# Performance work log

Hardware: AMD Instinct MI355X
Metric: run time of the kernel (lower is better)

## Reference

```python
import jax, jax.numpy as jnp
import numpy as np

N, E, FIN, H, G, L = 100000, 300000, 128, 256, 4000, 5
BN_EPS = 1e-5

def setup_inputs() -> dict:
    key = jax.random.key(0)
    ks = jax.random.split(key, 24)
    s = 0.05
    inp = {
        "x": jax.random.normal(ks[0], (N, FIN), dtype=jnp.float32),
        "edge_index": jax.random.randint(ks[1], (2, E), 0, N, dtype=jnp.int64),
        "batch": jnp.sort(jax.random.randint(ks[2], (N,), 0, G, dtype=jnp.int64)),
        # input projection
        "in_W": jax.random.normal(ks[3], (FIN, H), dtype=jnp.float32) * s,
        "in_b": jnp.zeros((H,), dtype=jnp.float32),
        # stacked per-layer GIN MLP params (Linear-BN-ReLU-Linear-BN-ReLU)
        "conv_W1": jax.random.normal(ks[4], (L, H, H), dtype=jnp.float32) * s,
        "conv_b1": jnp.zeros((L, H), dtype=jnp.float32),
        "conv_g1": jnp.ones((L, H), dtype=jnp.float32),
        "conv_be1": jnp.zeros((L, H), dtype=jnp.float32),
        "conv_W2": jax.random.normal(ks[5], (L, H, H), dtype=jnp.float32) * s,
        "conv_b2": jnp.zeros((L, H), dtype=jnp.float32),
        "conv_g2": jnp.ones((L, H), dtype=jnp.float32),
        "conv_be2": jnp.zeros((L, H), dtype=jnp.float32),
        "eps": jnp.zeros((L,), dtype=jnp.float32),
        # head MLP
        "head_W1": jax.random.normal(ks[6], (H, H // 2), dtype=jnp.float32) * s,
        "head_b1": jnp.zeros((H // 2,), dtype=jnp.float32),
        "head_W2": jax.random.normal(ks[7], (H // 2, 1), dtype=jnp.float32) * s,
        "head_b2": jnp.zeros((1,), dtype=jnp.float32),
    }
    return inp

def _bn(h, g, b):
    # BatchNorm1d over node dim (training-mode batch stats)
    m = jnp.mean(h, axis=0)
    v = jnp.var(h, axis=0)
    return g * (h - m) * jax.lax.rsqrt(v + BN_EPS) + b

def reference(x, edge_index, batch, in_W, in_b, conv_W1, conv_b1, conv_g1,
              conv_be1, conv_W2, conv_b2, conv_g2, conv_be2, eps,
              head_W1, head_b1, head_W2, head_b2):
    src, dst = edge_index[0], edge_index[1]
    h = jax.nn.relu(x @ in_W + in_b)  # [N,H]
    for l in range(L):
        agg = jax.ops.segment_sum(h[src], dst, num_segments=N)  # scatter-add
        z = (1.0 + eps[l]) * h + agg
        z = jax.nn.relu(_bn(z @ conv_W1[l] + conv_b1[l], conv_g1[l], conv_be1[l]))
        h = jax.nn.relu(_bn(z @ conv_W2[l] + conv_b2[l], conv_g2[l], conv_be2[l]))
        # dropout is identity in eval/reference
    # global mean pool by graph id
    sums = jax.ops.segment_sum(h, batch, num_segments=G)  # [G,H]
    cnt = jax.ops.segment_sum(jnp.ones((N,), h.dtype), batch, num_segments=G)
    pooled = sums / jnp.maximum(cnt, 1.0)[:, None]
    hid = jax.nn.relu(pooled @ head_W1 + head_b1)
    return hid @ head_W2 + head_b2  # [G,1]
```

## Files before the change

kernel.cpp:

```cpp
#include <hip/hip_runtime.h>
#include <hip/hip_bf16.h>
#include <stdint.h>
#include <stddef.h>

#define NN 100000
#define NE 300000
#define FINDIM 128
#define HD 256
#define NG 4000
#define NLAYER 5
#define MPAD 100096
#define NT (MPAD/32)
#define MG 384

typedef __attribute__((ext_vector_type(8))) short bf8;
typedef __attribute__((ext_vector_type(4))) float f4;

#define FENCE() __asm__ volatile("" ::: "memory")
#define WAITVM0() __asm__ volatile("s_waitcnt vmcnt(0)" ::: "memory")
#define WAITVM4() __asm__ volatile("s_waitcnt vmcnt(4)" ::: "memory")
#define WAITVM6() __asm__ volatile("s_waitcnt vmcnt(6)" ::: "memory")
#define WAITLGKM() __asm__ volatile("s_waitcnt lgkmcnt(0)" ::: "memory")
#define BARRIER() do { FENCE(); __builtin_amdgcn_s_barrier(); FENCE(); } while(0)

__device__ __forceinline__ unsigned short f2bf(float f){
  union { float f; unsigned u; } uf; uf.f = f;
  unsigned r = uf.u + 0x7fffu + ((uf.u >> 16) & 1u);
  return (unsigned short)(r >> 16);
}
__device__ __forceinline__ float bf2f(unsigned short h){
  union { unsigned u; float f; } uf; uf.u = ((unsigned)h) << 16; return uf.f;
}

__device__ __forceinline__ void gload16(const void* g, void* l){
  __builtin_amdgcn_global_load_lds((const __attribute__((address_space(1))) void*)g,
                                   (__attribute__((address_space(3))) void*)l, 16, 0, 0);
}

__global__ void k_zero(int* __restrict__ p, int n){
  int i = blockIdx.x*256 + threadIdx.x;
  if(i < n) p[i] = 0;
}

__global__ void k_count(const int* __restrict__ ei, int* __restrict__ counts){
  int e = blockIdx.x*256 + threadIdx.x;
  if(e < NE) atomicAdd(&counts[ei[NE + e]], 1);
}

__global__ void k_scan_partial(const int* __restrict__ counts, int* __restrict__ partials){
  __shared__ int sw[4];
  int b = blockIdx.x, t = threadIdx.x;
  int base = b*1024 + t*4;
  int s = 0;
  #pragma unroll
  for(int j=0;j<4;j++){ int i = base+j; if(i < NN) s += counts[i]; }
  #pragma unroll
  for(int d=1; d<64; d<<=1) s += __shfl_xor(s, d, 64);
  if((t & 63) == 0) sw[t>>6] = s;
  __syncthreads();
  if(t == 0) partials[b] = sw[0]+sw[1]+sw[2]+sw[3];
}

__global__ void k_scan_tot(int* __restrict__ partials, int* __restrict__ offsets, int nb){
  __shared__ int sm[128];
  int t = threadIdx.x;
  int v = (t < nb) ? partials[t] : 0;
  sm[t] = v; __syncthreads();
  for(int d=1; d<128; d<<=1){
    int x = 0;
    if(t >= d) x = sm[t-d];
    __syncthreads();
    sm[t] += x;
    __syncthreads();
  }
  if(t < nb) partials[t] = sm[t] - v;
  if(t == 127) offsets[NN] = sm[127];
}

__global__ void k_scan_final(const int* __restrict__ counts, const int* __restrict__ partials,
                             int* __restrict__ offsets, int* __restrict__ cursor){
  __shared__ int wsum[4];
  int b = blockIdx.x, t = threadIdx.x;
  int base = b*1024 + t*4;
  int c[4]; int ts = 0;
  #pragma unroll
  for(int j=0;j<4;j++){ int i = base+j; c[j] = (i < NN) ? counts[i] : 0; ts += c[j]; }
  int lane = t & 63;
  int inc = ts;
  #pragma unroll
  for(int d=1; d<64; d<<=1){ int x = __shfl_up(inc, d, 64); if(lane >= d) inc += x; }
  if(lane == 63) wsum[t>>6] = inc;
  __syncthreads();
  int woff = 0;
  for(int w2=0; w2<(t>>6); w2++) woff += wsum[w2];
  int excl = partials[b] + woff + inc - ts;
  #pragma unroll
  for(int j=0;j<4;j++){
    int i = base+j;
    if(i < NN){ offsets[i] = excl; cursor[i] = excl; excl += c[j]; }
  }
}

__global__ void k_fill(const int* __restrict__ ei, int* __restrict__ cursor, int* __restrict__ eidx){
  int e = blockIdx.x*256 + threadIdx.x;
  if(e < NE){
    int d = ei[NE + e];
    int pos = atomicAdd(&cursor[d], 1);
    eidx[pos] = ei[e];
  }
}

__global__ void k_wt(const float* __restrict__ src, unsigned short* __restrict__ dst, int K, int Ncols){
  int l = blockIdx.y;
  size_t base = (size_t)l * K * Ncols;
  int i = blockIdx.x*256 + threadIdx.x;
  if(i < K*Ncols){
    int k = i / Ncols, n = i % Ncols;
    dst[base + (size_t)n*K + k] = f2bf(src[base + i]);
  }
}

template<int TRANS, bool RELUOUT, bool STATS>
__global__ __launch_bounds__(256, 3) void k_gemmb(
    const unsigned short* __restrict__ A, const unsigned short* __restrict__ Bt,
    const float* __restrict__ bias, const float* __restrict__ preS,
    const float* __restrict__ preT, unsigned short* __restrict__ C,
    float* __restrict__ stats)
{
  __shared__ __align__(16) unsigned short As[2][8192];
  __shared__ __align__(16) unsigned short Cs[4][1152];
  __shared__ __align__(16) float SP[512];
  const int t = threadIdx.x;
  const int lane = t & 63, w = t >> 6;
  const int q = lane >> 4, ln = lane & 15;
  const int nh = blockIdx.x & 1;
  const int mg = blockIdx.x >> 1;
  const int nbase = nh*128 + w*32;

  if(TRANS){ SP[t] = preS[t]; SP[256 + t] = preT[t]; WAITLGKM(); }

  bf8 bb[2][8];
  #pragma unroll
  for(int nf=0; nf<2; nf++)
    #pragma unroll
    for(int s=0; s<8; s++)
      bb[nf][s] = *(const bf8*)(Bt + (size_t)(nbase + nf*16 + ln)*HD + s*32 + q*8);

  float bv[2];
  #pragma unroll
  for(int nf=0; nf<2; nf++) bv[nf] = bias[nbase + nf*16 + ln];

  auto issueA = [&](int mt, int b){
    const int m0 = mt*32;
    #pragma unroll
    for(int j=0; j<4; j++){
      int slot = j*256 + t;
      int row = slot >> 5, p = slot & 31;
      int c = p ^ (row & 7);
      gload16(A + (size_t)(m0 + row)*HD + c*8, &As[b][(j*256 + w*64)*8]);
    }
  };

  float sacc[2] = {0.f, 0.f}, ssacc[2] = {0.f, 0.f};

  issueA(mg, 0);
  issueA(mg + MG, 1);

  int tc = 0;
  for(int mt = mg; mt < NT; mt += MG, tc++){
    const bool last = (mt + MG >= NT);
    if(last)           WAITVM0();
    else if(tc == 0)   WAITVM4();
    else               WAITVM6();
    BARRIER();

    unsigned short* Ab = &As[tc&1][0];
    const int m0 = mt*32;
    const bool padt = (m0 >= NN);

    if(TRANS){
      #pragma unroll
      for(int j=0; j<4; j++){
        int slot = j*256 + t;
        if(padt){
          *(uint4*)&Ab[slot*8] = (uint4){0u,0u,0u,0u};
        } else {
          int row = slot >> 5, p = slot & 31;
          int c = p ^ (row & 7);
          uint4 u = *(const uint4*)&Ab[slot*8];
          f4 s0 = *(const f4*)&SP[c*8];
          f4 s1 = *(const f4*)&SP[c*8 + 4];
          f4 t0 = *(const f4*)&SP[256 + c*8];
          f4 t1 = *(const f4*)&SP[256 + c*8 + 4];
          float scv[8] = {s0.x,s0.y,s0.z,s0.w,s1.x,s1.y,s1.z,s1.w};
          float shv[8] = {t0.x,t0.y,t0.z,t0.w,t1.x,t1.y,t1.z,t1.w};
          unsigned short* us = (unsigned short*)&u;
          #pragma unroll
          for(int e=0; e<8; e++){
            float v = bf2f(us[e]);
            v = fmaxf(fmaf(scv[e], v, shv[e]), 0.f);
            us[e] = f2bf(v);
          }
          *(uint4*)&Ab[slot*8] = u;
        }
      }
      WAITLGKM();
      BARRIER();
    }

    f4 acc[2][2];
    #pragma unroll
    for(int i=0;i<2;i++)
      #pragma unroll
      for(int j=0;j<2;j++) acc[i][j] = (f4){0.f,0.f,0.f,0.f};

    #pragma unroll
    for(int s=0; s<8; s++){
      bf8 af[2];
      #pragma unroll
      for(int mi=0; mi<2; mi++){
        int row = mi*16 + ln;
        int p = (s*4 + q) ^ (row & 7);
        af[mi] = *(const bf8*)&Ab[row*256 + p*8];
      }
      #pragma unroll
      for(int mi=0; mi<2; mi++)
        #pragma unroll
        for(int nf=0; nf<2; nf++)
          acc[mi][nf] = __builtin_amdgcn_mfma_f32_16x16x32_bf16(af[mi], bb[nf][s], acc[mi][nf], 0, 0, 0);
    }

    if(STATS){
      #pragma unroll
      for(int nf=0; nf<2; nf++)
        #pragma unroll
        for(int mi=0; mi<2; mi++)
          #pragma unroll
          for(int r=0; r<4; r++){
            float v = acc[mi][nf][r];
            sacc[nf] += v; ssacc[nf] = fmaf(v, v, ssacc[nf]);
          }
    }

    unsigned short* wsc = &Cs[w][0];
    #pragma unroll
    for(int mi=0; mi<2; mi++)
      #pragma unroll
      for(int nf=0; nf<2; nf++)
        #pragma unroll
        for(int r=0; r<4; r++){
          float v = acc[mi][nf][r] + bv[nf];
          if(RELUOUT) v = fmaxf(v, 0.f);
          if(padt) v = 0.f;
          wsc[(mi*16 + q*4 + r)*36 + nf*16 + ln] = f2bf(v);
        }
    {
      int r2 = lane >> 1, ch = lane & 1;
      size_t cb = (size_t)(m0 + r2)*HD + nh*128 + w*32;
      uint4 u0 = *(const uint4*)&wsc[r2*36 + ch*8];
      uint4 u1 = *(const uint4*)&wsc[r2*36 + (ch+2)*8];
      *(uint4*)&C[cb + ch*8]     = u0;
      *(uint4*)&C[cb + (ch+2)*8] = u1;
    }

    WAITLGKM();
    BARRIER();
    if(mt + 2*MG < NT) issueA(mt + 2*MG, tc&1);
  }

  if(STATS){
    #pragma unroll
    for(int nf=0; nf<2; nf++){
      float s = sacc[nf], ss = ssacc[nf];
      s  += __shfl_xor(s, 16, 64);  s  += __shfl_xor(s, 32, 64);
      ss += __shfl_xor(ss, 16, 64); ss += __shfl_xor(ss, 32, 64);
      if(q == 0){
        int gn = nbase + nf*16 + ln;
        atomicAdd(&stats[gn], s);
        atomicAdd(&stats[HD + gn], ss);
      }
    }
  }
}

__global__ __launch_bounds__(256, 3) void k_gemmb_in(
    const float* __restrict__ A, const unsigned short* __restrict__ Bt,
    const float* __restrict__ bias, unsigned short* __restrict__ C)
{
  __shared__ __align__(16) unsigned short As[4096];
  __shared__ __align__(16) unsigned short Cs[4][1152];
  const int t = threadIdx.x;
  const int lane = t & 63, w = t >> 6;
  const int q = lane >> 4, ln = lane & 15;
  const int nh = blockIdx.x & 1;
  const int mg = blockIdx.x >> 1;
  const int nbase = nh*128 + w*32;

  bf8 bb[2][4];
  #pragma unroll
  for(int nf=0; nf<2; nf++)
    #pragma unroll
    for(int s=0; s<4; s++)
      bb[nf][s] = *(const bf8*)(Bt + (size_t)(nbase + nf*16 + ln)*FINDIM + s*32 + q*8);

  float bv[2];
  #pragma unroll
  for(int nf=0; nf<2; nf++) bv[nf] = bias[nbase + nf*16 + ln];

  for(int mt = mg; mt < NT; mt += MG){
    const int m0 = mt*32;
    const bool padt = (m0 >= NN);
    __syncthreads();
    #pragma unroll
    for(int j=0; j<2; j++){
      int slot = j*256 + t;
      int row = slot >> 4, p = slot & 15;
      int c = p ^ (row & 7);
      int gm = m0 + row;
      f4 v0 = (f4){0.f,0.f,0.f,0.f}, v1 = (f4){0.f,0.f,0.f,0.f};
      if(gm < NN){
        v0 = *(const f4*)&A[(size_t)gm*FINDIM + c*8];
        v1 = *(const f4*)&A[(size_t)gm*FINDIM + c*8 + 4];
      }
      ushort4 a0, a1;
      a0.x = f2bf(v0.x); a0.y = f2bf(v0.y); a0.z = f2bf(v0.z); a0.w = f2bf(v0.w);
      a1.x = f2bf(v1.x); a1.y = f2bf(v1.y); a1.z = f2bf(v1.z); a1.w = f2bf(v1.w);
      *(ushort4*)&As[row*128 + p*8]     = a0;
      *(ushort4*)&As[row*128 + p*8 + 4] = a1;
    }
    __syncthreads();

    f4 acc[2][2];
    #pragma unroll
    for(int i=0;i<2;i++)
      #pragma unroll
      for(int j=0;j<2;j++) acc[i][j] = (f4){0.f,0.f,0.f,0.f};

    #pragma unroll
    for(int s=0; s<4; s++){
      bf8 af[2];
      #pragma unroll
      for(int mi=0; mi<2; mi++){
        int row = mi*16 + ln;
        int p = (s*4 + q) ^ (row & 7);
        af[mi] = *(const bf8*)&As[row*128 + p*8];
      }
      #pragma unroll
      for(int mi=0; mi<2; mi++)
        #pragma unroll
        for(int nf=0; nf<2; nf++)
          acc[mi][nf] = __builtin_amdgcn_mfma_f32_16x16x32_bf16(af[mi], bb[nf][s], acc[mi][nf], 0, 0, 0);
    }

    unsigned short* wsc = &Cs[w][0];
    #pragma unroll
    for(int mi=0; mi<2; mi++)
      #pragma unroll
      for(int nf=0; nf<2; nf++)
        #pragma unroll
        for(int r=0; r<4; r++){
          float v = fmaxf(acc[mi][nf][r] + bv[nf], 0.f);
          if(padt) v = 0.f;
          wsc[(mi*16 + q*4 + r)*36 + nf*16 + ln] = f2bf(v);
        }
    int r2 = lane >> 1, ch = lane & 1;
    size_t cb = (size_t)(m0 + r2)*HD + nh*128 + w*32;
    uint4 u0 = *(const uint4*)&wsc[r2*36 + ch*8];
    uint4 u1 = *(const uint4*)&wsc[r2*36 + (ch+2)*8];
    *(uint4*)&C[cb + ch*8]     = u0;
    *(uint4*)&C[cb + (ch+2)*8] = u1;
  }
}

__global__ void k_bnfin(const float* __restrict__ cs, const float* __restrict__ bias,
                        const float* __restrict__ g, const float* __restrict__ be,
                        float* __restrict__ sc, float* __restrict__ sh){
  int c = threadIdx.x;
  float m0 = cs[c] * (1.0f/NN);
  float mean = m0 + bias[c];
  float var  = cs[HD + c] * (1.0f/NN) - m0*m0;
  float s = g[c] * rsqrtf(var + 1e-5f);
  sc[c] = s;
  sh[c] = be[c] - mean*s;
}

__device__ __forceinline__ f4 act4(ushort4 uv, f4 s4, f4 t4, int ident){
  f4 u;
  u.x = bf2f(uv.x); u.y = bf2f(uv.y); u.z = bf2f(uv.z); u.w = bf2f(uv.w);
  if(!ident){
    u.x = fmaxf(fmaf(s4.x, u.x, t4.x), 0.f);
    u.y = fmaxf(fmaf(s4.y, u.y, t4.y), 0.f);
    u.z = fmaxf(fmaf(s4.z, u.z, t4.z), 0.f);
    u.w = fmaxf(fmaf(s4.w, u.w, t4.w), 0.f);
  }
  return u;
}

__global__ __launch_bounds__(256) void k_agg(const unsigned short* __restrict__ src,
    unsigned short* __restrict__ dst,
    const int* __restrict__ offs, const int* __restrict__ eidx,
    const float* __restrict__ eps, int l,
    const float* __restrict__ sc, const float* __restrict__ sh, int ident)
{
  int wv = threadIdx.x >> 6;
  int n = blockIdx.x*4 + wv;
  if(n >= NN) return;
  int lane = threadIdx.x & 63;
  int c = lane << 2;
  f4 s4 = (f4){0.f,0.f,0.f,0.f}, t4 = (f4){0.f,0.f,0.f,0.f};
  if(!ident){ s4 = *(const f4*)(sc + c); t4 = *(const f4*)(sh + c); }
  float ep = 1.f + eps[l];
  f4 a = act4(*(const ushort4*)(src + (size_t)n*HD + c), s4, t4, ident);
  f4 acc;
  acc.x = ep*a.x; acc.y = ep*a.y; acc.z = ep*a.z; acc.w = ep*a.w;
  int lo = offs[n], hi = offs[n+1];
  for(int base = lo; base < hi; base += 64){
    int rem = hi - base; if(rem > 64) rem = 64;
    int idx = 0;
    if(base + lane < hi) idx = eidx[base + lane];
    int j = 0;
    for(; j + 4 <= rem; j += 4){
      int s0 = __shfl(idx, j, 64),   s1 = __shfl(idx, j+1, 64);
      int s2 = __shfl(idx, j+2, 64), s3 = __shfl(idx, j+3, 64);
      ushort4 u0 = *(const ushort4*)(src + (size_t)s0*HD + c);
      ushort4 u1 = *(const ushort4*)(src + (size_t)s1*HD + c);
      ushort4 u2 = *(const ushort4*)(src + (size_t)s2*HD + c);
      ushort4 u3 = *(const ushort4*)(src + (size_t)s3*HD + c);
      f4 a0 = act4(u0, s4, t4, ident), a1 = act4(u1, s4, t4, ident);
      f4 a2 = act4(u2, s4, t4, ident), a3 = act4(u3, s4, t4, ident);
      acc.x += (a0.x + a1.x) + (a2.x + a3.x);
      acc.y += (a0.y + a1.y) + (a2.y + a3.y);
      acc.z += (a0.z + a1.z) + (a2.z + a3.z);
      acc.w += (a0.w + a1.w) + (a2.w + a3.w);
    }
    for(; j < rem; j++){
      int s0 = __shfl(idx, j, 64);
      f4 a0 = act4(*(const ushort4*)(src + (size_t)s0*HD + c), s4, t4, ident);
      acc.x += a0.x; acc.y += a0.y; acc.z += a0.z; acc.w += a0.w;
    }
  }
  ushort4 o;
  o.x = f2bf(acc.x); o.y = f2bf(acc.y); o.z = f2bf(acc.z); o.w = f2bf(acc.w);
  *(ushort4*)(dst + (size_t)n*HD + c) = o;
}

__device__ __forceinline__ int lowb(const int* __restrict__ arr, int n, int key){
  int lo = 0, hi = n;
  while(lo < hi){ int mid = (lo + hi) >> 1; if(arr[mid] < key) lo = mid + 1; else hi = mid; }
  return lo;
}

__global__ __launch_bounds__(256) void k_pool(const unsigned short* __restrict__ src,
    const int* __restrict__ batch,
    const float* __restrict__ sc, const float* __restrict__ sh, float* __restrict__ pooled)
{
  int wv = threadIdx.x >> 6;
  int g = blockIdx.x*4 + wv;
  if(g >= NG) return;
  int lane = threadIdx.x & 63;
  int c = lane << 2;
  int lo = lowb(batch, NN, g);
  int hi = lowb(batch, NN, g+1);
  f4 s4 = *(const f4*)(sc + c);
  f4 t4 = *(const f4*)(sh + c);
  f4 acc = (f4){0.f,0.f,0.f,0.f};
  for(int n=lo; n<hi; n++){
    ushort4 uv = *(const ushort4*)(src + (size_t)n*HD + c);
    acc.x += fmaxf(fmaf(s4.x, bf2f(uv.x), t4.x), 0.f);
    acc.y += fmaxf(fmaf(s4.y, bf2f(uv.y), t4.y), 0.f);
    acc.z += fmaxf(fmaf(s4.z, bf2f(uv.z), t4.z), 0.f);
    acc.w += fmaxf(fmaf(s4.w, bf2f(uv.w), t4.w), 0.f);
  }
  float inv = 1.0f / fmaxf((float)(hi - lo), 1.0f);
  acc.x *= inv; acc.y *= inv; acc.z *= inv; acc.w *= inv;
  *(f4*)(pooled + (size_t)g*HD + c) = acc;
}

__global__ __launch_bounds__(128) void k_head(const float* __restrict__ pooled,
    const float* __restrict__ W1, const float* __restrict__ b1,
    const float* __restrict__ W2, const float* __restrict__ b2, float* __restrict__ out)
{
  __shared__ float p[HD];
  __shared__ float red[2];
  int g = blockIdx.x, t = threadIdx.x;
  if(t < 64) *(f4*)&p[t*4] = *(const f4*)(pooled + (size_t)g*HD + t*4);
  __syncthreads();
  float s = b1[t];
  for(int k=0;k<HD;k++) s = fmaf(p[k], W1[k*128 + t], s);
  float o = fmaxf(s, 0.f) * W2[t];
  #pragma unroll
  for(int d=1; d<64; d<<=1) o += __shfl_xor(o, d, 64);
  if((t & 63) == 0) red[t>>6] = o;
  __syncthreads();
  if(t == 0) out[g] = red[0] + red[1] + b2[0];
}

extern "C" void kernel_launch(void* const* d_in, const int* in_sizes, int n_in,
                              void* d_out, int out_size, void* d_ws, size_t ws_size,
                              hipStream_t stream) {
  const float* x    = (const float*)d_in[0];
  const int*   ei   = (const int*)  d_in[1];
  const int*   bat  = (const int*)  d_in[2];
  const float* inW  = (const float*)d_in[3];
  const float* inb  = (const float*)d_in[4];
  const float* W1   = (const float*)d_in[5];
  const float* b1   = (const float*)d_in[6];
  const float* g1   = (const float*)d_in[7];
  const float* be1  = (const float*)d_in[8];
  const float* W2   = (const float*)d_in[9];
  const float* b2   = (const float*)d_in[10];
  const float* g2   = (const float*)d_in[11];
  const float* be2  = (const float*)d_in[12];
  const float* eps  = (const float*)d_in[13];
  const float* hW1  = (const float*)d_in[14];
  const float* hb1  = (const float*)d_in[15];
  const float* hW2  = (const float*)d_in[16];
  const float* hb2  = (const float*)d_in[17];
  float* out = (float*)d_out;

  char* p = (char*)d_ws;
  auto alloc = [&](size_t bytes)->char*{
    char* r = p; p += (bytes + 255) & ~(size_t)255; return r;
  };
  unsigned short* B0 = (unsigned short*)alloc((size_t)MPAD*HD*2);
  unsigned short* B1 = (unsigned short*)alloc((size_t)MPAD*HD*2);
  unsigned short* Wtin = (unsigned short*)alloc((size_t)FINDIM*HD*2);
  unsigned short* Wt1  = (unsigned short*)alloc((size_t)NLAYER*HD*HD*2);
  unsigned short* Wt2  = (unsigned short*)alloc((size_t)NLAYER*HD*HD*2);
  int* counts  = (int*)alloc((size_t)NN*4);
  int* offsets = (int*)alloc((size_t)(NN+1)*4);
  int* cursor  = (int*)alloc((size_t)NN*4);
  int* eidx    = (int*)alloc((size_t)NE*4);
  int* partials= (int*)alloc(128*4);
  float* cs    = (float*)alloc(4*HD*4);
  float* bnp   = (float*)alloc(4*HD*4);
  float* pooled= (float*)alloc((size_t)NG*HD*4);

  k_zero<<<(NN+255)/256, 256, 0, stream>>>(counts, NN);
  k_count<<<(NE+255)/256, 256, 0, stream>>>(ei, counts);
  int nb = (NN + 1023)/1024;
  k_scan_partial<<<nb, 256, 0, stream>>>(counts, partials);
  k_scan_tot<<<1, 128, 0, stream>>>(partials, offsets, nb);
  k_scan_final<<<nb, 256, 0, stream>>>(counts, partials, offsets, cursor);
  k_fill<<<(NE+255)/256, 256, 0, stream>>>(ei, cursor, eidx);

  k_wt<<<dim3((FINDIM*HD+255)/256, 1), 256, 0, stream>>>(inW, Wtin, FINDIM, HD);
  k_wt<<<dim3((HD*HD+255)/256, NLAYER), 256, 0, stream>>>(W1, Wt1, HD, HD);
  k_wt<<<dim3((HD*HD+255)/256, NLAYER), 256, 0, stream>>>(W2, Wt2, HD, HD);

  {
    int padInts = (MPAD - NN) * HD / 2;
    k_zero<<<(padInts+255)/256, 256, 0, stream>>>((int*)(B1 + (size_t)NN*HD), padInts);
  }

  k_gemmb_in<<<2*MG, 256, 0, stream>>>(x, Wtin, inb, B0);

  float* sc1 = bnp, *sh1 = bnp + HD, *sc2 = bnp + 2*HD, *sh2 = bnp + 3*HD;
  unsigned short* hbuf = B0;
  unsigned short* tbuf = B1;
  for(int l=0; l<NLAYER; l++){
    k_zero<<<4, 256, 0, stream>>>((int*)cs, 4*HD);
    k_agg<<<(NN+3)/4, 256, 0, stream>>>(hbuf, tbuf, offsets, eidx, eps, l, sc2, sh2, l==0 ? 1 : 0);
    k_gemmb<0, false, true><<<2*MG, 256, 0, stream>>>(tbuf, Wt1 + (size_t)l*HD*HD, b1 + l*HD,
                                                      nullptr, nullptr, hbuf, cs);
    k_bnfin<<<1, HD, 0, stream>>>(cs, b1 + l*HD, g1 + l*HD, be1 + l*HD, sc1, sh1);
    k_gemmb<1, false, true><<<2*MG, 256, 0, stream>>>(hbuf, Wt2 + (size_t)l*HD*HD, b2 + l*HD,
                                                      sc1, sh1, tbuf, cs + 2*HD);
    k_bnfin<<<1, HD, 0, stream>>>(cs + 2*HD, b2 + l*HD, g2 + l*HD, be2 + l*HD, sc2, sh2);
    unsigned short* tmp = hbuf; hbuf = tbuf; tbuf = tmp;
  }

  k_pool<<<(NG+3)/4, 256, 0, stream>>>(hbuf, bat, sc2, sh2, pooled);
  k_head<<<NG, 128, 0, stream>>>(pooled, hW1, hb1, hW2, hb2, out);
}
```

Baseline: 840.5 us.

## Fuse neighbor aggregation into first GIN GEMM with gathered LDS tiles

Replaces the separate aggregation kernel and first per-layer GEMM with one kernel that gathers neighbor rows, applies the pending BN+ReLU, sums with (1+eps)·self, and writes the bf16 tile straight into shared memory. An MFMA GEMM over the full 256 output columns then runs on that tile, with 512-thread blocks and the whole weight slice held in registers. This removes the write and reread of the aggregated activation buffer in every layer. The cost is that the irregular gather latency now sits inside the GEMM loop, overlapped only by double buffering, and the larger register footprint may lower occupancy. The buffer ping-pong is replaced by fixed B0/B1 roles.

```diff
diff --git a/kernel.cpp b/kernel.cpp
--- a/kernel.cpp
+++ b/kernel.cpp
@@ -11,7 +11,8 @@
 #define NLAYER 5
 #define MPAD 100096
 #define NT (MPAD/32)
-#define MG 384
+#define MGB 384
+#define MGF 512
 
 typedef __attribute__((ext_vector_type(8))) short bf8;
 typedef __attribute__((ext_vector_type(4))) float f4;
@@ -117,6 +118,178 @@
   if(i < K*Ncols){
     int k = i / Ncols, n = i % Ncols;
     dst[base + (size_t)n*K + k] = f2bf(src[base + i]);
+  }
+}
+
+__device__ __forceinline__ f4 act4(ushort4 uv, f4 s4, f4 t4, int ident){
+  f4 u;
+  u.x = bf2f(uv.x); u.y = bf2f(uv.y); u.z = bf2f(uv.z); u.w = bf2f(uv.w);
+  if(!ident){
+    u.x = fmaxf(fmaf(s4.x, u.x, t4.x), 0.f);
+    u.y = fmaxf(fmaf(s4.y, u.y, t4.y), 0.f);
+    u.z = fmaxf(fmaf(s4.z, u.z, t4.z), 0.f);
+    u.w = fmaxf(fmaf(s4.w, u.w, t4.w), 0.f);
+  }
+  return u;
+}
+
+template<int IDENT>
+__global__ __launch_bounds__(512) void k_gfuse(
+    const unsigned short* __restrict__ h, const unsigned short* __restrict__ Bt,
+    const float* __restrict__ bias, const float* __restrict__ sc,
+    const float* __restrict__ sh, const float* __restrict__ eps, int l,
+    const int* __restrict__ offs, const int* __restrict__ eidx,
+    unsigned short* __restrict__ C, float* __restrict__ stats)
+{
+  __shared__ __align__(16) unsigned short As[2][8192];
+  __shared__ __align__(16) unsigned short Cs[8][1152];
+  const int t = threadIdx.x;
+  const int lane = t & 63, w = t >> 6;
+  const int q = lane >> 4, ln = lane & 15;
+  const int mg = blockIdx.x;
+  const int nbase = w*32;
+  const int gc = lane*4;
+
+  f4 s4 = (f4){0.f,0.f,0.f,0.f}, t4 = (f4){0.f,0.f,0.f,0.f};
+  if(!IDENT){ s4 = *(const f4*)(sc + gc); t4 = *(const f4*)(sh + gc); }
+  const float ep = 1.f + eps[l];
+
+  bf8 bb[2][8];
+  #pragma unroll
+  for(int nf=0; nf<2; nf++)
+    #pragma unroll
+    for(int s=0; s<8; s++)
+      bb[nf][s] = *(const bf8*)(Bt + (size_t)(nbase + nf*16 + ln)*HD + s*32 + q*8);
+
+  float bv[2];
+  #pragma unroll
+  for(int nf=0; nf<2; nf++) bv[nf] = bias[nbase + nf*16 + ln];
+
+  auto gather = [&](int mt, int b){
+    unsigned short* Ab = &As[b][0];
+    const int m0 = mt*32;
+    if(m0 >= NN){
+      *(uint4*)&Ab[t*16]     = (uint4){0u,0u,0u,0u};
+      *(uint4*)&Ab[t*16 + 8] = (uint4){0u,0u,0u,0u};
+      return;
+    }
+    #pragma unroll
+    for(int rr=0; rr<4; rr++){
+      const int r = w*4 + rr;
+      const int n = m0 + r;
+      f4 a = act4(*(const ushort4*)(h + (size_t)n*HD + gc), s4, t4, IDENT);
+      f4 acc;
+      acc.x = ep*a.x; acc.y = ep*a.y; acc.z = ep*a.z; acc.w = ep*a.w;
+      int lo = offs[n], hi = offs[n+1];
+      for(int base = lo; base < hi; base += 64){
+        int rem = hi - base; if(rem > 64) rem = 64;
+        int idxv = 0;
+        if(base + lane < hi) idxv = eidx[base + lane];
+        int j = 0;
+        for(; j + 4 <= rem; j += 4){
+          int s0 = __shfl(idxv, j, 64),   s1 = __shfl(idxv, j+1, 64);
+          int s2 = __shfl(idxv, j+2, 64), s3 = __shfl(idxv, j+3, 64);
+          ushort4 u0 = *(const ushort4*)(h + (size_t)s0*HD + gc);
+          ushort4 u1 = *(const ushort4*)(h + (size_t)s1*HD + gc);
+          ushort4 u2 = *(const ushort4*)(h + (size_t)s2*HD + gc);
+          ushort4 u3 = *(const ushort4*)(h + (size_t)s3*HD + gc);
+          f4 a0 = act4(u0, s4, t4, IDENT), a1 = act4(u1, s4, t4, IDENT);
+          f4 a2 = act4(u2, s4, t4, IDENT), a3 = act4(u3, s4, t4, IDENT);
+          acc.x += (a0.x + a1.x) + (a2.x + a3.x);
+          acc.y += (a0.y + a1.y) + (a2.y + a3.y);
+          acc.z += (a0.z + a1.z) + (a2.z + a3.z);
+          acc.w += (a0.w + a1.w) + (a2.w + a3.w);
+        }
+        for(; j < rem; j++){
+          int s0 = __shfl(idxv, j, 64);
+          f4 a0 = act4(*(const ushort4*)(h + (size_t)s0*HD + gc), s4, t4, IDENT);
+          acc.x += a0.x; acc.y += a0.y; acc.z += a0.z; acc.w += a0.w;
+        }
+      }
+      ushort4 o;
+      o.x = f2bf(acc.x); o.y = f2bf(acc.y); o.z = f2bf(acc.z); o.w = f2bf(acc.w);
+      int p = (lane >> 1) ^ (r & 7);
+      *(ushort4*)&Ab[r*256 + p*8 + (lane & 1)*4] = o;
+    }
+  };
+
+  float sacc[2] = {0.f, 0.f}, ssacc[2] = {0.f, 0.f};
+
+  gather(mg, 0);
+  __syncthreads();
+
+  int tc = 0;
+  for(int mt = mg; mt < NT; mt += MGF, tc++){
+    const unsigned short* Ab = &As[tc&1][0];
+    const int m0 = mt*32;
+    const bool padt = (m0 >= NN);
+
+    f4 acc[2][2];
+    #pragma unroll
+    for(int i=0;i<2;i++)
+      #pragma unroll
+      for(int j=0;j<2;j++) acc[i][j] = (f4){0.f,0.f,0.f,0.f};
+
+    #pragma unroll
+    for(int s=0; s<8; s++){
+      bf8 af[2];
+      #pragma unroll
+      for(int mi=0; mi<2; mi++){
+        int row = mi*16 + ln;
+        int p = (s*4 + q) ^ (row & 7);
+        af[mi] = *(const bf8*)&Ab[row*256 + p*8];
+      }
+      #pragma unroll
+      for(int mi=0; mi<2; mi++)
+        #pragma unroll
+        for(int nf=0; nf<2; nf++)
+          acc[mi][nf] = __builtin_amdgcn_mfma_f32_16x16x32_bf16(af[mi], bb[nf][s], acc[mi][nf], 0, 0, 0);
+    }
+
+    #pragma unroll
+    for(int nf=0; nf<2; nf++)
+      #pragma unroll
+      for(int mi=0; mi<2; mi++)
+        #pragma unroll
+        for(int r=0; r<4; r++){
+          float v = acc[mi][nf][r];
+          sacc[nf] += v; ssacc[nf] = fmaf(v, v, ssacc[nf]);
+        }
+
+    unsigned short* wsc = &Cs[w][0];
+    #pragma unroll
+    for(int mi=0; mi<2; mi++)
+      #pragma unroll
+      for(int nf=0; nf<2; nf++)
+        #pragma unroll
+        for(int r=0; r<4; r++){
+          float v = acc[mi][nf][r] + bv[nf];
+          if(padt) v = 0.f;
+          wsc[(mi*16 + q*4 + r)*36 + nf*16 + ln] = f2bf(v);
+        }
+    {
+      int r2 = lane >> 1, ch = lane & 1;
+      size_t cb = (size_t)(m0 + r2)*HD + w*32;
+      uint4 u0 = *(const uint4*)&wsc[r2*36 + ch*8];
+      uint4 u1 = *(const uint4*)&wsc[r2*36 + (ch+2)*8];
+      *(uint4*)&C[cb + ch*8]     = u0;
+      *(uint4*)&C[cb + (ch+2)*8] = u1;
+    }
+
+    if(mt + MGF < NT) gather(mt + MGF, (tc+1)&1);
+    __syncthreads();
+  }
+
+  #pragma unroll
+  for(int nf=0; nf<2; nf++){
+    float s = sacc[nf], ss = ssacc[nf];
+    s  += __shfl_xor(s, 16, 64);  s  += __shfl_xor(s, 32, 64);
+    ss += __shfl_xor(ss, 16, 64); ss += __shfl_xor(ss, 32, 64);
+    if(q == 0){
+      int gn = nbase + nf*16 + ln;
+      atomicAdd(&stats[gn], s);
+      atomicAdd(&stats[HD + gn], ss);
+    }
   }
 }
 
@@ -164,11 +337,11 @@
   float sacc[2] = {0.f, 0.f}, ssacc[2] = {0.f, 0.f};
 
   issueA(mg, 0);
-  issueA(mg + MG, 1);
+  issueA(mg + MGB, 1);
 
   int tc = 0;
-  for(int mt = mg; mt < NT; mt += MG, tc++){
-    const bool last = (mt + MG >= NT);
+  for(int mt = mg; mt < NT; mt += MGB, tc++){
+    const bool last = (mt + MGB >= NT);
     if(last)           WAITVM0();
     else if(tc == 0)   WAITVM4();
     else               WAITVM6();
@@ -265,7 +438,7 @@
 
     WAITLGKM();
     BARRIER();
-    if(mt + 2*MG < NT) issueA(mt + 2*MG, tc&1);
+    if(mt + 2*MGB < NT) issueA(mt + 2*MGB, tc&1);
   }
 
   if(STATS){
@@ -307,7 +480,7 @@
   #pragma unroll
   for(int nf=0; nf<2; nf++) bv[nf] = bias[nbase + nf*16 + ln];
 
-  for(int mt = mg; mt < NT; mt += MG){
+  for(int mt = mg; mt < NT; mt += MGB){
     const int m0 = mt*32;
     const bool padt = (m0 >= NN);
     __syncthreads();
@@ -382,66 +555,6 @@
   float s = g[c] * rsqrtf(var + 1e-5f);
   sc[c] = s;
   sh[c] = be[c] - mean*s;
-}
-
-__device__ __forceinline__ f4 act4(ushort4 uv, f4 s4, f4 t4, int ident){
-  f4 u;
-  u.x = bf2f(uv.x); u.y = bf2f(uv.y); u.z = bf2f(uv.z); u.w = bf2f(uv.w);
-  if(!ident){
-    u.x = fmaxf(fmaf(s4.x, u.x, t4.x), 0.f);
-    u.y = fmaxf(fmaf(s4.y, u.y, t4.y), 0.f);
-    u.z = fmaxf(fmaf(s4.z, u.z, t4.z), 0.f);
-    u.w = fmaxf(fmaf(s4.w, u.w, t4.w), 0.f);
-  }
-  return u;
-}
-
-__global__ __launch_bounds__(256) void k_agg(const unsigned short* __restrict__ src,
-    unsigned short* __restrict__ dst,
-    const int* __restrict__ offs, const int* __restrict__ eidx,
-    const float* __restrict__ eps, int l,
-    const float* __restrict__ sc, const float* __restrict__ sh, int ident)
-{
-  int wv = threadIdx.x >> 6;
-  int n = blockIdx.x*4 + wv;
-  if(n >= NN) return;
-  int lane = threadIdx.x & 63;
-  int c = lane << 2;
-  f4 s4 = (f4){0.f,0.f,0.f,0.f}, t4 = (f4){0.f,0.f,0.f,0.f};
-  if(!ident){ s4 = *(const f4*)(sc + c); t4 = *(const f4*)(sh + c); }
-  float ep = 1.f + eps[l];
-  f4 a = act4(*(const ushort4*)(src + (size_t)n*HD + c), s4, t4, ident);
-  f4 acc;
-  acc.x = ep*a.x; acc.y = ep*a.y; acc.z = ep*a.z; acc.w = ep*a.w;
-  int lo = offs[n], hi = offs[n+1];
-  for(int base = lo; base < hi; base += 64){
-    int rem = hi - base; if(rem > 64) rem = 64;
-    int idx = 0;
-    if(base + lane < hi) idx = eidx[base + lane];
-    int j = 0;
-    for(; j + 4 <= rem; j += 4){
-      int s0 = __shfl(idx, j, 64),   s1 = __shfl(idx, j+1, 64);
-      int s2 = __shfl(idx, j+2, 64), s3 = __shfl(idx, j+3, 64);
-      ushort4 u0 = *(const ushort4*)(src + (size_t)s0*HD + c);
-      ushort4 u1 = *(const ushort4*)(src + (size_t)s1*HD + c);
-      ushort4 u2 = *(const ushort4*)(src + (size_t)s2*HD + c);
-      ushort4 u3 = *(const ushort4*)(src + (size_t)s3*HD + c);
-      f4 a0 = act4(u0, s4, t4, ident), a1 = act4(u1, s4, t4, ident);
-      f4 a2 = act4(u2, s4, t4, ident), a3 = act4(u3, s4, t4, ident);
-      acc.x += (a0.x + a1.x) + (a2.x + a3.x);
-      acc.y += (a0.y + a1.y) + (a2.y + a3.y);
-      acc.z += (a0.z + a1.z) + (a2.z + a3.z);
-      acc.w += (a0.w + a1.w) + (a2.w + a3.w);
-    }
-    for(; j < rem; j++){
-      int s0 = __shfl(idx, j, 64);
-      f4 a0 = act4(*(const ushort4*)(src + (size_t)s0*HD + c), s4, t4, ident);
-      acc.x += a0.x; acc.y += a0.y; acc.z += a0.z; acc.w += a0.w;
-    }
-  }
-  ushort4 o;
-  o.x = f2bf(acc.x); o.y = f2bf(acc.y); o.z = f2bf(acc.z); o.w = f2bf(acc.w);
-  *(ushort4*)(dst + (size_t)n*HD + c) = o;
 }
 
 __device__ __forceinline__ int lowb(const int* __restrict__ arr, int n, int key){
@@ -553,23 +666,23 @@
     k_zero<<<(padInts+255)/256, 256, 0, stream>>>((int*)(B1 + (size_t)NN*HD), padInts);
   }
 
-  k_gemmb_in<<<2*MG, 256, 0, stream>>>(x, Wtin, inb, B0);
+  k_gemmb_in<<<2*MGB, 256, 0, stream>>>(x, Wtin, inb, B0);
 
   float* sc1 = bnp, *sh1 = bnp + HD, *sc2 = bnp + 2*HD, *sh2 = bnp + 3*HD;
-  unsigned short* hbuf = B0;
-  unsigned short* tbuf = B1;
   for(int l=0; l<NLAYER; l++){
     k_zero<<<4, 256, 0, stream>>>((int*)cs, 4*HD);
-    k_agg<<<(NN+3)/4, 256, 0, stream>>>(hbuf, tbuf, offsets, eidx, eps, l, sc2, sh2, l==0 ? 1 : 0);
-    k_gemmb<0, false, true><<<2*MG, 256, 0, stream>>>(tbuf, Wt1 + (size_t)l*HD*HD, b1 + l*HD,
-                                                      nullptr, nullptr, hbuf, cs);
+    if(l == 0)
+      k_gfuse<1><<<MGF, 512, 0, stream>>>(B0, Wt1 + (size_t)l*HD*HD, b1 + l*HD,
+                                          sc2, sh2, eps, l, offsets, eidx, B1, cs);
+    else
+      k_gfuse<0><<<MGF, 512, 0, stream>>>(B0, Wt1 + (size_t)l*HD*HD, b1 + l*HD,
+                                          sc2, sh2, eps, l, offsets, eidx, B1, cs);
     k_bnfin<<<1, HD, 0, stream>>>(cs, b1 + l*HD, g1 + l*HD, be1 + l*HD, sc1, sh1);
-    k_gemmb<1, false, true><<<2*MG, 256, 0, stream>>>(hbuf, Wt2 + (size_t)l*HD*HD, b2 + l*HD,
-                                                      sc1, sh1, tbuf, cs + 2*HD);
+    k_gemmb<1, false, true><<<2*MGB, 256, 0, stream>>>(B1, Wt2 + (size_t)l*HD*HD, b2 + l*HD,
+                                                       sc1, sh1, B0, cs + 2*HD);
     k_bnfin<<<1, HD, 0, stream>>>(cs + 2*HD, b2 + l*HD, g2 + l*HD, be2 + l*HD, sc2, sh2);
-    unsigned short* tmp = hbuf; hbuf = tbuf; tbuf = tmp;
-  }
-
-  k_pool<<<(NG+3)/4, 256, 0, stream>>>(hbuf, bat, sc2, sh2, pooled);
+  }
+
+  k_pool<<<(NG+3)/4, 256, 0, stream>>>(B0, bat, sc2, sh2, pooled);
   k_head<<<NG, 128, 0, stream>>>(pooled, hW1, hb1, hW2, hb2, out);
 }
```

Measured after the change: 1.012 ms. +20.4%, slower.
